# Performance work log

Measured on AMD Instinct MI355X. Metric: run time of the kernel, lower is better.

## Reference

```python
import math
import jax, jax.numpy as jnp
import numpy as np

SIZE = 1.0            # scene cube extent; positions live in [-SIZE/2, SIZE/2]
N_LEVELS = 16         # number of hash-grid resolutions
TABLE_SIZE = 524288   # 2**19 entries per level
FEAT_DIM = 2          # features per entry
N_POINTS = 262144     # query points (rays * samples)
BASE_RES, MAX_RES = 16, 512

_PRIMES = jnp.array([1, 2654435761, 805459861], dtype=jnp.uint32)
# 8 corner offsets of a voxel, [8,3]
_OFFS = jnp.array([[(c >> 2) & 1, (c >> 1) & 1, c & 1] for c in range(8)], dtype=jnp.uint32)


def _level_lookup(xyz01, table, res):
    # xyz01: [N,3] in [0,1); table: [T,F]; res: scalar int32
    x = xyz01 * res.astype(xyz01.dtype)          # [N,3] grid coords
    x0f = jnp.floor(x)
    w = x - x0f                                  # [N,3] trilinear fracs
    x0 = x0f.astype(jnp.uint32)
    corners = x0[:, None, :] + _OFFS[None]       # [N,8,3]
    h = corners * _PRIMES                        # uint32 wraparound multiply
    idx = (h[..., 0] ^ h[..., 1] ^ h[..., 2]) % jnp.uint32(TABLE_SIZE)  # [N,8]
    feats = table[idx]                           # [N,8,F] gather
    ws = jnp.prod(jnp.where(_OFFS[None] == 1, w[:, None, :], 1.0 - w[:, None, :]), axis=-1)  # [N,8]
    return jnp.einsum('nc,ncf->nf', ws, feats)   # [N,F]


def _forward(xyz, tables, resolutions):
    # xyz: [N,3] in scene coords; tables: [L,T,F]; resolutions: [L] int32
    xyz01 = jnp.clip(xyz / SIZE + 0.5, 0.0, 1.0 - 1e-6)
    per_level = jax.vmap(_level_lookup, in_axes=(None, 0, 0))(xyz01, tables, resolutions)  # [L,N,F]
    return jnp.transpose(per_level, (1, 0, 2)).reshape(xyz.shape[0], N_LEVELS * FEAT_DIM)


def setup_inputs() -> dict:
    key = jax.random.key(0)
    k1, k2 = jax.random.split(key)
    xyz = (jax.random.uniform(k1, (N_POINTS, 3), dtype=jnp.float32) - 0.5) * SIZE
    tables = jax.random.normal(k2, (N_LEVELS, TABLE_SIZE, FEAT_DIM), dtype=jnp.float32) * 1e-2
    growth = (MAX_RES / BASE_RES) ** (1.0 / (N_LEVELS - 1))
    res = np.round(BASE_RES * growth ** np.arange(N_LEVELS)).astype(np.int32)
    return {"xyz": xyz, "tables": tables, "resolutions": jnp.array(res)}


def reference(xyz, tables, resolutions):
    return _forward(xyz, tables, resolutions)
```

## Files before the change

### kernel.cpp

```cpp
#include <hip/hip_runtime.h>


#define HG_N_LEVELS   16
#define HG_TABLE_SIZE 524288u
#define HG_TABLE_MASK (HG_TABLE_SIZE - 1u)

typedef float vf2 __attribute__((ext_vector_type(2)));
typedef float vf4 __attribute__((ext_vector_type(4)));

__device__ __forceinline__ void hg_prep2(
    float px, float py, float pz, float res,
    unsigned* __restrict__ s, float* __restrict__ wyz,
    unsigned* __restrict__ x0out, float* __restrict__ wx)
{
    const float lim = 1.0f - 1e-6f;
    float ux = fminf(fmaxf(px + 0.5f, 0.0f), lim);
    float uy = fminf(fmaxf(py + 0.5f, 0.0f), lim);
    float uz = fminf(fmaxf(pz + 0.5f, 0.0f), lim);
    float fx = ux * res, fy = uy * res, fz = uz * res;
    float x0f = floorf(fx), y0f = floorf(fy), z0f = floorf(fz);
    float wx1 = fx - x0f, wy1 = fy - y0f, wz1 = fz - z0f;
    float wx0 = 1.0f - wx1, wy0 = 1.0f - wy1, wz0 = 1.0f - wz1;
    unsigned x0 = (unsigned)x0f, y0 = (unsigned)y0f, z0 = (unsigned)z0f;
    const unsigned P1 = 2654435761u, P2 = 805459861u;
    unsigned hy0 = y0 * P1, hy1 = (y0 + 1u) * P1;
    unsigned hz0 = z0 * P2, hz1 = (z0 + 1u) * P2;
    s[0] = hy0 ^ hz0;  wyz[0] = wy0 * wz0;
    s[1] = hy0 ^ hz1;  wyz[1] = wy0 * wz1;
    s[2] = hy1 ^ hz0;  wyz[2] = wy1 * wz0;
    s[3] = hy1 ^ hz1;  wyz[3] = wy1 * wz1;
    *x0out = x0; wx[0] = wx0; wx[1] = wx1;
}

__device__ __forceinline__ void hg_prep(
    float px, float py, float pz, float res,
    unsigned* __restrict__ idx, float* __restrict__ w)
{
    unsigned s[4]; float wyz[4], wx[2]; unsigned x0;
    hg_prep2(px, py, pz, res, s, wyz, &x0, wx);
    #pragma unroll
    for (int j = 0; j < 4; ++j) {
        idx[j]     = (x0 ^ s[j]) & HG_TABLE_MASK;        w[j]     = wx[0] * wyz[j];
        idx[4 + j] = ((x0 + 1u) ^ s[j]) & HG_TABLE_MASK; w[4 + j] = wx[1] * wyz[j];
    }
}

__global__ __launch_bounds__(256) void hashgrid_gather_lvl(
    const float* __restrict__ xyz,
    const float* __restrict__ tables,
    const int*   __restrict__ resolutions,
    float*       __restrict__ ws,
    int n_points)
{
    const int x    = blockIdx.x & 7;
    const int slot = blockIdx.x >> 3;
    const int C    = (n_points + 511) >> 9;
    const int C8   = (C + 7) >> 3;

    int level, chunk;
    if (slot < C)            { level = 8 + x; chunk = slot; }
    else if (slot < C + C8)  { int j = slot - C; level = 7; chunk = x + (j << 3); }
    else                     { int j = slot - C - C8;
                               if (x >= 6) { level = 6; chunk = (x - 6) + (j << 1); }
                               else        { level = x; chunk = j; } }
    if (chunk >= C) return;

    const float res = (float)resolutions[level];
    const float2* __restrict__ tbl =
        (const float2*)tables + (size_t)level * HG_TABLE_SIZE;
    float* __restrict__ wlev = ws + (size_t)level * n_points * 2;

    const int p0 = (chunk << 9) + ((int)threadIdx.x << 1);
    if (p0 >= n_points) return;

    if (p0 + 1 < n_points) {
        const float* xp = xyz + (size_t)p0 * 3;
        vf2 c0 = *(const vf2*)(xp);
        vf2 c1 = *(const vf2*)(xp + 2);
        vf2 c2 = *(const vf2*)(xp + 4);

        unsigned sA[4], sB[4], x0A, x0B;
        float wyzA[4], wyzB[4], wxA[2], wxB[2];
        hg_prep2(c0.x, c0.y, c1.x, res, sA, wyzA, &x0A, wxA);
        hg_prep2(c1.y, c2.x, c2.y, res, sB, wyzB, &x0B, wxB);

        unsigned iA0[4], iA1[4], iB0[4], iB1[4];
        #pragma unroll
        for (int j = 0; j < 4; ++j) {
            iA0[j] = (x0A ^ sA[j]) & HG_TABLE_MASK;
            iA1[j] = ((x0A + 1u) ^ sA[j]) & HG_TABLE_MASK;
            iB0[j] = (x0B ^ sB[j]) & HG_TABLE_MASK;
            iB1[j] = ((x0B + 1u) ^ sB[j]) & HG_TABLE_MASK;
        }
        const bool oddA = (x0A & 1u) != 0u;
        const bool oddB = (x0B & 1u) != 0u;

        vf4 qA[4], qB[4];
        #pragma unroll
        for (int j = 0; j < 4; ++j) qA[j] = *(const vf4*)(tbl + (iA0[j] & ~1u));
        #pragma unroll
        for (int j = 0; j < 4; ++j) qB[j] = *(const vf4*)(tbl + (iB0[j] & ~1u));

        vf2 eA[4], eB[4];
        #pragma unroll
        for (int j = 0; j < 4; ++j) { eA[j] = (vf2)(0.f); eB[j] = (vf2)(0.f); }
        if (oddA) {
            #pragma unroll
            for (int j = 0; j < 4; ++j) eA[j] = *(const vf2*)(tbl + iA1[j]);
        }
        if (oddB) {
            #pragma unroll
            for (int j = 0; j < 4; ++j) eB[j] = *(const vf2*)(tbl + iB1[j]);
        }

        asm volatile(""
            : "+v"(qA[0]), "+v"(qA[1]), "+v"(qA[2]), "+v"(qA[3]),
              "+v"(qB[0]), "+v"(qB[1]), "+v"(qB[2]), "+v"(qB[3]),
              "+v"(eA[0]), "+v"(eA[1]), "+v"(eA[2]), "+v"(eA[3]),
              "+v"(eB[0]), "+v"(eB[1]), "+v"(eB[2]), "+v"(eB[3])
            :
            : "memory");

        float oax = 0.f, oay = 0.f, obx = 0.f, oby = 0.f;
        #pragma unroll
        for (int j = 0; j < 4; ++j) {
            bool hi = (iA0[j] & 1u) != 0u;
            vf2 lo; lo.x = qA[j].x; lo.y = qA[j].y;
            vf2 hiv; hiv.x = qA[j].z; hiv.y = qA[j].w;
            vf2 f0 = hi ? hiv : lo;
            vf2 f1 = oddA ? eA[j] : (hi ? lo : hiv);
            float w0 = wxA[0] * wyzA[j], w1 = wxA[1] * wyzA[j];
            oax += w0 * f0.x + w1 * f1.x;
            oay += w0 * f0.y + w1 * f1.y;
        }
        #pragma unroll
        for (int j = 0; j < 4; ++j) {
            bool hi = (iB0[j] & 1u) != 0u;
            vf2 lo; lo.x = qB[j].x; lo.y = qB[j].y;
            vf2 hiv; hiv.x = qB[j].z; hiv.y = qB[j].w;
            vf2 f0 = hi ? hiv : lo;
            vf2 f1 = oddB ? eB[j] : (hi ? lo : hiv);
            float w0 = wxB[0] * wyzB[j], w1 = wxB[1] * wyzB[j];
            obx += w0 * f0.x + w1 * f1.x;
            oby += w0 * f0.y + w1 * f1.y;
        }

        vf4 v; v.x = oax; v.y = oay; v.z = obx; v.w = oby;
        __builtin_nontemporal_store(v, (vf4*)(wlev + 2 * (size_t)p0));
    } else {
        float px = xyz[(size_t)p0 * 3 + 0];
        float py = xyz[(size_t)p0 * 3 + 1];
        float pz = xyz[(size_t)p0 * 3 + 2];
        unsigned idx[8]; float w[8];
        hg_prep(px, py, pz, res, idx, w);
        vf2 f[8];
        #pragma unroll
        for (int k = 0; k < 8; ++k) f[k] = *(const vf2*)(tbl + idx[k]);
        float sx = 0.f, sy = 0.f;
        #pragma unroll
        for (int k = 0; k < 8; ++k) { sx += w[k] * f[k].x; sy += w[k] * f[k].y; }
        vf2 v; v.x = sx; v.y = sy;
        __builtin_nontemporal_store(v, (vf2*)(wlev + 2 * (size_t)p0));
    }
}

#define TP_PTS 256
#define TP_STRIDE (2 * TP_PTS + 4)

__global__ __launch_bounds__(256) void hashgrid_transpose(
    const float* __restrict__ ws,
    float*       __restrict__ out,
    int n_points)
{
    __shared__ float tile[16 * TP_STRIDE];
    const int p0 = blockIdx.x * TP_PTS;
    const int t  = (int)threadIdx.x;
    const int npts = min(TP_PTS, n_points - p0);

    #pragma unroll
    for (int it = 0; it < 8; ++it) {
        int r  = it * 2 + (t >> 7);
        int q  = t & 127;
        int pt = q * 2;
        if (pt < npts) {
            const float* src = ws + (size_t)r * n_points * 2 + (size_t)(p0 + pt) * 2;
            vf4 v;
            if (pt + 1 < npts) v = *(const vf4*)src;
            else { vf2 v2 = *(const vf2*)src; v.x = v2.x; v.y = v2.y; v.z = 0.f; v.w = 0.f; }
            *(vf4*)&tile[r * TP_STRIDE + 4 * q] = v;
        }
    }
    __syncthreads();

    #pragma unroll
    for (int it = 0; it < 8; ++it) {
        int linear = it * 256 + t;
        int pt = linear >> 3;
        int v4 = linear & 7;
        if (pt < npts) {
            vf4 v;
            #pragma unroll
            for (int k = 0; k < 4; ++k) {
                int e = 4 * v4 + k;
                int lev = e >> 1, f = e & 1;
                v[k] = tile[lev * TP_STRIDE + 2 * pt + f];
            }
            __builtin_nontemporal_store(
                v, (vf4*)(out + (size_t)(p0 + pt) * 32 + 4 * v4));
        }
    }
}

__global__ __launch_bounds__(256) void hashgrid_fwd(
    const float* __restrict__ xyz,
    const float* __restrict__ tables,
    const int*   __restrict__ resolutions,
    float*       __restrict__ out,
    int n_points)
{
    int tid   = blockIdx.x * blockDim.x + threadIdx.x;
    int point = tid >> 4;
    int level = tid & 15;
    if (point >= n_points) return;

    float px = xyz[point * 3 + 0];
    float py = xyz[point * 3 + 1];
    float pz = xyz[point * 3 + 2];
    float res = (float)resolutions[level];
    const float2* __restrict__ tbl =
        (const float2*)tables + (size_t)level * HG_TABLE_SIZE;

    unsigned idx[8]; float w[8];
    hg_prep(px, py, pz, res, idx, w);
    vf2 f[8];
    #pragma unroll
    for (int k = 0; k < 8; ++k) f[k] = *(const vf2*)(tbl + idx[k]);
    float ox = 0.f, oy = 0.f;
    #pragma unroll
    for (int k = 0; k < 8; ++k) { ox += w[k] * f[k].x; oy += w[k] * f[k].y; }
    vf2 v; v.x = ox; v.y = oy;
    *(vf2*)(out + (size_t)point * 32 + 2 * level) = v;
}

extern "C" void kernel_launch(void* const* d_in, const int* in_sizes, int n_in,
                              void* d_out, int out_size, void* d_ws, size_t ws_size,
                              hipStream_t stream) {
    const float* xyz         = (const float*)d_in[0];
    const float* tables      = (const float*)d_in[1];
    const int*   resolutions = (const int*)d_in[2];
    float*       out         = (float*)d_out;

    int n_points = in_sizes[0] / 3;
    size_t ws_needed = (size_t)n_points * HG_N_LEVELS * sizeof(float2);

    if (ws_size >= ws_needed) {
        float* ws = (float*)d_ws;
        int C  = (n_points + 511) >> 9;
        int C8 = (C + 7) >> 3;
        int slots = 2 * C + C8;
        hashgrid_gather_lvl<<<8 * slots, 256, 0, stream>>>(
            xyz, tables, resolutions, ws, n_points);
        int tblocks = (n_points + TP_PTS - 1) / TP_PTS;
        hashgrid_transpose<<<tblocks, 256, 0, stream>>>(ws, out, n_points);
    } else {
        int n_threads = n_points * HG_N_LEVELS;
        hashgrid_fwd<<<(n_threads + 255) / 256, 256, 0, stream>>>(
            xyz, tables, resolutions, out, n_points);
    }
}
```

Baseline: 219.9 us.

## Split levels across two passes and fuse transpose into second gather pass

Replaces the gather-all-levels-then-transpose pipeline with two gather kernels: the first computes odd levels into a half-size workspace, and the second computes even levels and writes each (even, odd) level pair directly into the interleaved output using the workspace values. This removes the separate LDS transpose kernel and halves workspace traffic. In exchange, each pass only holds 8 levels in flight, so the earlier load-balanced level/chunk scheduling is dropped. Output writes are now 16-byte strided per point rather than fully coalesced rows.

```diff
diff --git a/kernel.cpp b/kernel.cpp
--- a/kernel.cpp
+++ b/kernel.cpp
@@ -45,30 +45,111 @@
     }
 }
 
-__global__ __launch_bounds__(256) void hashgrid_gather_lvl(
+__device__ __forceinline__ vf4 hg_gather2(
+    const float2* __restrict__ tbl, float res,
+    float ax, float ay, float az, float bx, float by, float bz)
+{
+    unsigned sA[4], sB[4], x0A, x0B;
+    float wyzA[4], wyzB[4], wxA[2], wxB[2];
+    hg_prep2(ax, ay, az, res, sA, wyzA, &x0A, wxA);
+    hg_prep2(bx, by, bz, res, sB, wyzB, &x0B, wxB);
+
+    unsigned iA0[4], iA1[4], iB0[4], iB1[4];
+    #pragma unroll
+    for (int j = 0; j < 4; ++j) {
+        iA0[j] = (x0A ^ sA[j]) & HG_TABLE_MASK;
+        iA1[j] = ((x0A + 1u) ^ sA[j]) & HG_TABLE_MASK;
+        iB0[j] = (x0B ^ sB[j]) & HG_TABLE_MASK;
+        iB1[j] = ((x0B + 1u) ^ sB[j]) & HG_TABLE_MASK;
+    }
+    const bool oddA = (x0A & 1u) != 0u;
+    const bool oddB = (x0B & 1u) != 0u;
+
+    vf4 qA[4], qB[4];
+    #pragma unroll
+    for (int j = 0; j < 4; ++j) qA[j] = *(const vf4*)(tbl + (iA0[j] & ~1u));
+    #pragma unroll
+    for (int j = 0; j < 4; ++j) qB[j] = *(const vf4*)(tbl + (iB0[j] & ~1u));
+
+    vf2 eA[4], eB[4];
+    #pragma unroll
+    for (int j = 0; j < 4; ++j) { eA[j] = (vf2)(0.f); eB[j] = (vf2)(0.f); }
+    if (oddA) {
+        #pragma unroll
+        for (int j = 0; j < 4; ++j) eA[j] = *(const vf2*)(tbl + iA1[j]);
+    }
+    if (oddB) {
+        #pragma unroll
+        for (int j = 0; j < 4; ++j) eB[j] = *(const vf2*)(tbl + iB1[j]);
+    }
+
+    asm volatile(""
+        : "+v"(qA[0]), "+v"(qA[1]), "+v"(qA[2]), "+v"(qA[3]),
+          "+v"(qB[0]), "+v"(qB[1]), "+v"(qB[2]), "+v"(qB[3]),
+          "+v"(eA[0]), "+v"(eA[1]), "+v"(eA[2]), "+v"(eA[3]),
+          "+v"(eB[0]), "+v"(eB[1]), "+v"(eB[2]), "+v"(eB[3])
+        :
+        : "memory");
+
+    float oax = 0.f, oay = 0.f, obx = 0.f, oby = 0.f;
+    #pragma unroll
+    for (int j = 0; j < 4; ++j) {
+        bool hi = (iA0[j] & 1u) != 0u;
+        vf2 lo;  lo.x  = qA[j].x; lo.y  = qA[j].y;
+        vf2 hiv; hiv.x = qA[j].z; hiv.y = qA[j].w;
+        vf2 f0 = hi ? hiv : lo;
+        vf2 f1 = oddA ? eA[j] : (hi ? lo : hiv);
+        float w0 = wxA[0] * wyzA[j], w1 = wxA[1] * wyzA[j];
+        oax += w0 * f0.x + w1 * f1.x;
+        oay += w0 * f0.y + w1 * f1.y;
+    }
+    #pragma unroll
+    for (int j = 0; j < 4; ++j) {
+        bool hi = (iB0[j] & 1u) != 0u;
+        vf2 lo;  lo.x  = qB[j].x; lo.y  = qB[j].y;
+        vf2 hiv; hiv.x = qB[j].z; hiv.y = qB[j].w;
+        vf2 f0 = hi ? hiv : lo;
+        vf2 f1 = oddB ? eB[j] : (hi ? lo : hiv);
+        float w0 = wxB[0] * wyzB[j], w1 = wxB[1] * wyzB[j];
+        obx += w0 * f0.x + w1 * f1.x;
+        oby += w0 * f0.y + w1 * f1.y;
+    }
+
+    vf4 r; r.x = oax; r.y = oay; r.z = obx; r.w = oby;
+    return r;
+}
+
+__device__ __forceinline__ vf2 hg_gather1(
+    const float2* __restrict__ tbl, float res,
+    float px, float py, float pz)
+{
+    unsigned idx[8]; float w[8];
+    hg_prep(px, py, pz, res, idx, w);
+    vf2 f[8];
+    #pragma unroll
+    for (int k = 0; k < 8; ++k) f[k] = *(const vf2*)(tbl + idx[k]);
+    float sx = 0.f, sy = 0.f;
+    #pragma unroll
+    for (int k = 0; k < 8; ++k) { sx += w[k] * f[k].x; sy += w[k] * f[k].y; }
+    vf2 v; v.x = sx; v.y = sy;
+    return v;
+}
+
+__global__ __launch_bounds__(256) void hashgrid_pa(
     const float* __restrict__ xyz,
     const float* __restrict__ tables,
     const int*   __restrict__ resolutions,
     float*       __restrict__ ws,
     int n_points)
 {
-    const int x    = blockIdx.x & 7;
-    const int slot = blockIdx.x >> 3;
-    const int C    = (n_points + 511) >> 9;
-    const int C8   = (C + 7) >> 3;
-
-    int level, chunk;
-    if (slot < C)            { level = 8 + x; chunk = slot; }
-    else if (slot < C + C8)  { int j = slot - C; level = 7; chunk = x + (j << 3); }
-    else                     { int j = slot - C - C8;
-                               if (x >= 6) { level = 6; chunk = (x - 6) + (j << 1); }
-                               else        { level = x; chunk = j; } }
-    if (chunk >= C) return;
+    const int x     = blockIdx.x & 7;
+    const int chunk = blockIdx.x >> 3;
+    const int level = 2 * x + 1;
 
     const float res = (float)resolutions[level];
     const float2* __restrict__ tbl =
         (const float2*)tables + (size_t)level * HG_TABLE_SIZE;
-    float* __restrict__ wlev = ws + (size_t)level * n_points * 2;
+    float* __restrict__ wrow = ws + (size_t)x * n_points * 2;
 
     const int p0 = (chunk << 9) + ((int)threadIdx.x << 1);
     if (p0 >= n_points) return;
@@ -78,136 +159,60 @@
         vf2 c0 = *(const vf2*)(xp);
         vf2 c1 = *(const vf2*)(xp + 2);
         vf2 c2 = *(const vf2*)(xp + 4);
-
-        unsigned sA[4], sB[4], x0A, x0B;
-        float wyzA[4], wyzB[4], wxA[2], wxB[2];
-        hg_prep2(c0.x, c0.y, c1.x, res, sA, wyzA, &x0A, wxA);
-        hg_prep2(c1.y, c2.x, c2.y, res, sB, wyzB, &x0B, wxB);
-
-        unsigned iA0[4], iA1[4], iB0[4], iB1[4];
-        #pragma unroll
-        for (int j = 0; j < 4; ++j) {
-            iA0[j] = (x0A ^ sA[j]) & HG_TABLE_MASK;
-            iA1[j] = ((x0A + 1u) ^ sA[j]) & HG_TABLE_MASK;
-            iB0[j] = (x0B ^ sB[j]) & HG_TABLE_MASK;
-            iB1[j] = ((x0B + 1u) ^ sB[j]) & HG_TABLE_MASK;
-        }
-        const bool oddA = (x0A & 1u) != 0u;
-        const bool oddB = (x0B & 1u) != 0u;
-
-        vf4 qA[4], qB[4];
-        #pragma unroll
-        for (int j = 0; j < 4; ++j) qA[j] = *(const vf4*)(tbl + (iA0[j] & ~1u));
-        #pragma unroll
-        for (int j = 0; j < 4; ++j) qB[j] = *(const vf4*)(tbl + (iB0[j] & ~1u));
-
-        vf2 eA[4], eB[4];
-        #pragma unroll
-        for (int j = 0; j < 4; ++j) { eA[j] = (vf2)(0.f); eB[j] = (vf2)(0.f); }
-        if (oddA) {
-            #pragma unroll
-            for (int j = 0; j < 4; ++j) eA[j] = *(const vf2*)(tbl + iA1[j]);
-        }
-        if (oddB) {
-            #pragma unroll
-            for (int j = 0; j < 4; ++j) eB[j] = *(const vf2*)(tbl + iB1[j]);
-        }
-
-        asm volatile(""
-            : "+v"(qA[0]), "+v"(qA[1]), "+v"(qA[2]), "+v"(qA[3]),
-              "+v"(qB[0]), "+v"(qB[1]), "+v"(qB[2]), "+v"(qB[3]),
-              "+v"(eA[0]), "+v"(eA[1]), "+v"(eA[2]), "+v"(eA[3]),
-              "+v"(eB[0]), "+v"(eB[1]), "+v"(eB[2]), "+v"(eB[3])
-            :
-            : "memory");
-
-        float oax = 0.f, oay = 0.f, obx = 0.f, oby = 0.f;
-        #pragma unroll
-        for (int j = 0; j < 4; ++j) {
-            bool hi = (iA0[j] & 1u) != 0u;
-            vf2 lo; lo.x = qA[j].x; lo.y = qA[j].y;
-            vf2 hiv; hiv.x = qA[j].z; hiv.y = qA[j].w;
-            vf2 f0 = hi ? hiv : lo;
-            vf2 f1 = oddA ? eA[j] : (hi ? lo : hiv);
-            float w0 = wxA[0] * wyzA[j], w1 = wxA[1] * wyzA[j];
-            oax += w0 * f0.x + w1 * f1.x;
-            oay += w0 * f0.y + w1 * f1.y;
-        }
-        #pragma unroll
-        for (int j = 0; j < 4; ++j) {
-            bool hi = (iB0[j] & 1u) != 0u;
-            vf2 lo; lo.x = qB[j].x; lo.y = qB[j].y;
-            vf2 hiv; hiv.x = qB[j].z; hiv.y = qB[j].w;
-            vf2 f0 = hi ? hiv : lo;
-            vf2 f1 = oddB ? eB[j] : (hi ? lo : hiv);
-            float w0 = wxB[0] * wyzB[j], w1 = wxB[1] * wyzB[j];
-            obx += w0 * f0.x + w1 * f1.x;
-            oby += w0 * f0.y + w1 * f1.y;
-        }
-
-        vf4 v; v.x = oax; v.y = oay; v.z = obx; v.w = oby;
-        __builtin_nontemporal_store(v, (vf4*)(wlev + 2 * (size_t)p0));
+        vf4 v = hg_gather2(tbl, res, c0.x, c0.y, c1.x, c1.y, c2.x, c2.y);
+        __builtin_nontemporal_store(v, (vf4*)(wrow + 2 * (size_t)p0));
     } else {
-        float px = xyz[(size_t)p0 * 3 + 0];
-        float py = xyz[(size_t)p0 * 3 + 1];
-        float pz = xyz[(size_t)p0 * 3 + 2];
-        unsigned idx[8]; float w[8];
-        hg_prep(px, py, pz, res, idx, w);
-        vf2 f[8];
-        #pragma unroll
-        for (int k = 0; k < 8; ++k) f[k] = *(const vf2*)(tbl + idx[k]);
-        float sx = 0.f, sy = 0.f;
-        #pragma unroll
-        for (int k = 0; k < 8; ++k) { sx += w[k] * f[k].x; sy += w[k] * f[k].y; }
-        vf2 v; v.x = sx; v.y = sy;
-        __builtin_nontemporal_store(v, (vf2*)(wlev + 2 * (size_t)p0));
-    }
-}
-
-#define TP_PTS 256
-#define TP_STRIDE (2 * TP_PTS + 4)
-
-__global__ __launch_bounds__(256) void hashgrid_transpose(
+        vf2 v = hg_gather1(tbl, res,
+                           xyz[(size_t)p0 * 3 + 0],
+                           xyz[(size_t)p0 * 3 + 1],
+                           xyz[(size_t)p0 * 3 + 2]);
+        __builtin_nontemporal_store(v, (vf2*)(wrow + 2 * (size_t)p0));
+    }
+}
+
+__global__ __launch_bounds__(256) void hashgrid_pb(
+    const float* __restrict__ xyz,
+    const float* __restrict__ tables,
+    const int*   __restrict__ resolutions,
     const float* __restrict__ ws,
     float*       __restrict__ out,
     int n_points)
 {
-    __shared__ float tile[16 * TP_STRIDE];
-    const int p0 = blockIdx.x * TP_PTS;
-    const int t  = (int)threadIdx.x;
-    const int npts = min(TP_PTS, n_points - p0);
-
-    #pragma unroll
-    for (int it = 0; it < 8; ++it) {
-        int r  = it * 2 + (t >> 7);
-        int q  = t & 127;
-        int pt = q * 2;
-        if (pt < npts) {
-            const float* src = ws + (size_t)r * n_points * 2 + (size_t)(p0 + pt) * 2;
-            vf4 v;
-            if (pt + 1 < npts) v = *(const vf4*)src;
-            else { vf2 v2 = *(const vf2*)src; v.x = v2.x; v.y = v2.y; v.z = 0.f; v.w = 0.f; }
-            *(vf4*)&tile[r * TP_STRIDE + 4 * q] = v;
-        }
-    }
-    __syncthreads();
-
-    #pragma unroll
-    for (int it = 0; it < 8; ++it) {
-        int linear = it * 256 + t;
-        int pt = linear >> 3;
-        int v4 = linear & 7;
-        if (pt < npts) {
-            vf4 v;
-            #pragma unroll
-            for (int k = 0; k < 4; ++k) {
-                int e = 4 * v4 + k;
-                int lev = e >> 1, f = e & 1;
-                v[k] = tile[lev * TP_STRIDE + 2 * pt + f];
-            }
-            __builtin_nontemporal_store(
-                v, (vf4*)(out + (size_t)(p0 + pt) * 32 + 4 * v4));
-        }
+    const int x     = blockIdx.x & 7;
+    const int chunk = blockIdx.x >> 3;
+    const int level = 2 * x;
+
+    const float res = (float)resolutions[level];
+    const float2* __restrict__ tbl =
+        (const float2*)tables + (size_t)level * HG_TABLE_SIZE;
+    const float* __restrict__ wrow = ws + (size_t)x * n_points * 2;
+
+    const int p0 = (chunk << 9) + ((int)threadIdx.x << 1);
+    if (p0 >= n_points) return;
+
+    if (p0 + 1 < n_points) {
+        vf4 wsv = __builtin_nontemporal_load((const vf4*)(wrow + 2 * (size_t)p0));
+        asm volatile("" : "+v"(wsv));
+
+        const float* xp = xyz + (size_t)p0 * 3;
+        vf2 c0 = *(const vf2*)(xp);
+        vf2 c1 = *(const vf2*)(xp + 2);
+        vf2 c2 = *(const vf2*)(xp + 4);
+        vf4 g = hg_gather2(tbl, res, c0.x, c0.y, c1.x, c1.y, c2.x, c2.y);
+
+        vf4 o0; o0.x = g.x; o0.y = g.y; o0.z = wsv.x; o0.w = wsv.y;
+        vf4 o1; o1.x = g.z; o1.y = g.w; o1.z = wsv.z; o1.w = wsv.w;
+        float* op = out + (size_t)p0 * 32 + 4 * x;
+        __builtin_nontemporal_store(o0, (vf4*)op);
+        __builtin_nontemporal_store(o1, (vf4*)(op + 32));
+    } else {
+        vf2 wsv = __builtin_nontemporal_load((const vf2*)(wrow + 2 * (size_t)p0));
+        vf2 g = hg_gather1(tbl, res,
+                           xyz[(size_t)p0 * 3 + 0],
+                           xyz[(size_t)p0 * 3 + 1],
+                           xyz[(size_t)p0 * 3 + 2]);
+        vf4 o; o.x = g.x; o.y = g.y; o.z = wsv.x; o.w = wsv.y;
+        __builtin_nontemporal_store(o, (vf4*)(out + (size_t)p0 * 32 + 4 * x));
     }
 }
 
@@ -230,15 +235,7 @@
     const float2* __restrict__ tbl =
         (const float2*)tables + (size_t)level * HG_TABLE_SIZE;
 
-    unsigned idx[8]; float w[8];
-    hg_prep(px, py, pz, res, idx, w);
-    vf2 f[8];
-    #pragma unroll
-    for (int k = 0; k < 8; ++k) f[k] = *(const vf2*)(tbl + idx[k]);
-    float ox = 0.f, oy = 0.f;
-    #pragma unroll
-    for (int k = 0; k < 8; ++k) { ox += w[k] * f[k].x; oy += w[k] * f[k].y; }
-    vf2 v; v.x = ox; v.y = oy;
+    vf2 v = hg_gather1(tbl, res, px, py, pz);
     *(vf2*)(out + (size_t)point * 32 + 2 * level) = v;
 }
 
@@ -251,17 +248,15 @@
     float*       out         = (float*)d_out;
 
     int n_points = in_sizes[0] / 3;
-    size_t ws_needed = (size_t)n_points * HG_N_LEVELS * sizeof(float2);
+    size_t ws_needed = (size_t)n_points * 8 * sizeof(float2);
 
     if (ws_size >= ws_needed) {
         float* ws = (float*)d_ws;
-        int C  = (n_points + 511) >> 9;
-        int C8 = (C + 7) >> 3;
-        int slots = 2 * C + C8;
-        hashgrid_gather_lvl<<<8 * slots, 256, 0, stream>>>(
+        int C = (n_points + 511) >> 9;
+        hashgrid_pa<<<8 * C, 256, 0, stream>>>(
             xyz, tables, resolutions, ws, n_points);
-        int tblocks = (n_points + TP_PTS - 1) / TP_PTS;
-        hashgrid_transpose<<<tblocks, 256, 0, stream>>>(ws, out, n_points);
+        hashgrid_pb<<<8 * C, 256, 0, stream>>>(
+            xyz, tables, resolutions, ws, out, n_points);
     } else {
         int n_threads = n_points * HG_N_LEVELS;
         hashgrid_fwd<<<(n_threads + 255) / 256, 256, 0, stream>>>(
```

Result: slower. 231.6 us (+5.3%).
